# Performance work log

Hardware: AMD Instinct MI355X
Metric: run time of the kernel (lower is better)

Reference implementation:

```python
import jax, jax.numpy as jnp
import numpy as np

DROPOUT_P = 0.9  # module's self.dropout_p, training=True by default
DROPOUT_KEY = 42  # fixed key for deterministic reference


def setup_inputs() -> dict:
    key = jax.random.key(0)
    kq, kk, kv = jax.random.split(key, 3)
    B, H, S, D = 4, 16, 2048, 64
    q = jax.random.normal(kq, (B, H, S, D), dtype=jnp.float32)
    k = jax.random.normal(kk, (B, H, S, D), dtype=jnp.float32)
    v = jax.random.normal(kv, (B, H, S, D), dtype=jnp.float32)
    return {"q": q, "k": k, "v": v}


def reference(q, k, v):
    # qk = q @ k^T  -> [B,H,Sq,Skv]
    qk = jnp.einsum("bhqd,bhkd->bhqk", q, k)
    # NOTE: module divides by v.size(-1)**-0.5, i.e. multiplies by sqrt(Dv)
    inv_scale_factor = v.shape[-1] ** (-0.5)
    scaled_qk = qk / inv_scale_factor
    softmax_qk = jax.nn.softmax(scaled_qk, axis=-1)
    # dropout with p=0.9, training=True; fixed key for determinism
    keep = jax.random.bernoulli(jax.random.key(DROPOUT_KEY), 1.0 - DROPOUT_P, softmax_qk.shape)
    dropout_qk = jnp.where(keep, softmax_qk / (1.0 - DROPOUT_P), 0.0)
    out = jnp.einsum("bhqk,bhkd->bhqd", dropout_qk, v)
    return out
```

## Files before the change

### kernel.cpp

```cpp
#include <hip/hip_runtime.h>


typedef short short8 __attribute__((ext_vector_type(8)));
typedef float floatx4 __attribute__((ext_vector_type(4)));

#define S_LEN 2048
#define D_DIM 64
#define BM 64
#define BN 64
#define NTILES (S_LEN / BN)
#define E_THR 1e-7f
#define MARG 2.025f
#define CAND_CAP 40
#define K_ELEMS (64 * S_LEN * D_DIM)
#define WS_NEEDED ((size_t)K_ELEMS * 4)
#define TILE_BYTES 16384
#define BH_BYTES (NTILES * TILE_BYTES)

__device__ __forceinline__ unsigned int rotl32(unsigned int x, int n) {
  return (x << n) | (x >> (32 - n));
}

__device__ __forceinline__ unsigned int threefry_42_xorfold(unsigned int idx) {
  const unsigned int ks1 = 42u, ks2 = 0x1BD11BF0u;
  unsigned int x0 = 0u;
  unsigned int x1 = idx + ks1;
#define TF4(a, b, c, d)                          \
  x0 += x1; x1 = rotl32(x1, a); x1 ^= x0;        \
  x0 += x1; x1 = rotl32(x1, b); x1 ^= x0;        \
  x0 += x1; x1 = rotl32(x1, c); x1 ^= x0;        \
  x0 += x1; x1 = rotl32(x1, d); x1 ^= x0;
  TF4(13, 15, 26, 6)
  x0 += ks1; x1 += ks2 + 1u;
  TF4(17, 29, 16, 24)
  x0 += ks2; x1 += 2u;
  TF4(13, 15, 26, 6)
  x1 += ks1 + 3u;
  TF4(17, 29, 16, 24)
  x0 += ks1; x1 += ks2 + 4u;
  TF4(13, 15, 26, 6)
  x0 += ks2; x1 += 5u;
#undef TF4
  return x0 ^ x1;
}

__device__ __forceinline__ void split4(float4 x, uint2* hp, uint2* lop) {
  const unsigned int u0 = __float_as_uint(x.x), u1 = __float_as_uint(x.y);
  const unsigned int u2 = __float_as_uint(x.z), u3 = __float_as_uint(x.w);
  hp->x = (u0 >> 16) | (u1 & 0xFFFF0000u);
  hp->y = (u2 >> 16) | (u3 & 0xFFFF0000u);
  const float l0 = x.x - __uint_as_float(u0 & 0xFFFF0000u);
  const float l1 = x.y - __uint_as_float(u1 & 0xFFFF0000u);
  const float l2 = x.z - __uint_as_float(u2 & 0xFFFF0000u);
  const float l3 = x.w - __uint_as_float(u3 & 0xFFFF0000u);
  lop->x = (__float_as_uint(l0) >> 16) | (__float_as_uint(l1) & 0xFFFF0000u);
  lop->y = (__float_as_uint(l2) >> 16) | (__float_as_uint(l3) & 0xFFFF0000u);
}

__device__ __forceinline__ void split8(const float* x, short8* hi, short8* lo) {
  union { short8 s; uint2 u[2]; } h, l;
  split4(*(const float4*)(x + 0), &h.u[0], &l.u[0]);
  split4(*(const float4*)(x + 4), &h.u[1], &l.u[1]);
  *hi = h.s; *lo = l.s;
}

__global__ void split_k_kernel(const float* __restrict__ k, unsigned char* __restrict__ ws) {
  const int c = blockIdx.x * 256 + threadIdx.x;
  const int bh = c >> 14;
  const int cc = c & 16383;
  const int srow = cc >> 3, col8 = cc & 7;
  const int tile = srow >> 6, row = srow & 63;
  const float* src = k + ((size_t)bh * S_LEN + srow) * D_DIM + col8 * 8;
  float b8[8];
  *(float4*)&b8[0] = *(const float4*)src;
  *(float4*)&b8[4] = *(const float4*)(src + 4);
  short8 h, l;
  split8(b8, &h, &l);
  unsigned char* dst = ws + (size_t)bh * BH_BYTES + tile * TILE_BYTES +
                       row * 128 + ((col8 * 16) ^ ((row & 7) << 4));
  *(short8*)dst = h;
  *(short8*)(dst + 8192) = l;
}

__global__ __launch_bounds__(256, 4) void attn_dropout_kernel(
    const float* __restrict__ q, const float* __restrict__ k,
    const float* __restrict__ v, float* __restrict__ out,
    const unsigned char* __restrict__ kws, int usews) {
  __shared__ uint4 Kbuf[1024];
  __shared__ float2 cand[BM][CAND_CAP];
  __shared__ int cnt[BM];
  __shared__ float rowm8[BM];

  const int t = threadIdx.x;
  const int w = t >> 6;
  const int m16 = t & 15;
  const int qd = (t & 63) >> 4;
  const int lane = t & 63;
  const int i0 = blockIdx.x * BM;
  const int bh = blockIdx.y;

  const float* Qg = q + ((size_t)bh * S_LEN + i0) * D_DIM;
  const float* Kg = k + (size_t)bh * S_LEN * D_DIM;
  const float* Vg = v + (size_t)bh * S_LEN * D_DIM;

  if (t < BM) cnt[t] = 0;

  short8 ah0, ah1, al0, al1;
  {
    const int arow = 16 * w + m16;
    float qbuf[8];
    *(float4*)&qbuf[0] = *(const float4*)(Qg + arow * D_DIM + qd * 8);
    *(float4*)&qbuf[4] = *(const float4*)(Qg + arow * D_DIM + qd * 8 + 4);
    split8(qbuf, &ah0, &al0);
    *(float4*)&qbuf[0] = *(const float4*)(Qg + arow * D_DIM + 32 + qd * 8);
    *(float4*)&qbuf[4] = *(const float4*)(Qg + arow * D_DIM + 32 + qd * 8 + 4);
    split8(qbuf, &ah1, &al1);
  }

  float mrow[4];
#pragma unroll
  for (int r = 0; r < 4; ++r) mrow[r] = -1e30f;

  const unsigned int bh_base = (unsigned int)bh * (unsigned int)(S_LEN * S_LEN);

  const int swz = (m16 & 7) << 4;
  const int b_lo = m16 * 128 + ((qd * 16) ^ swz);
  const int b_hi = m16 * 128 + ((qd * 16 + 64) ^ swz);

  auto compute_tile = [&](int j0) {
    const char* Kb = (const char*)&Kbuf[0];
    floatx4 acc[4];
#pragma unroll
    for (int jj = 0; jj < 4; ++jj) {
      short8 kh0 = *(const short8*)(Kb + jj * 2048 + b_lo);
      short8 kh1 = *(const short8*)(Kb + jj * 2048 + b_hi);
      short8 kl0 = *(const short8*)(Kb + 8192 + jj * 2048 + b_lo);
      short8 kl1 = *(const short8*)(Kb + 8192 + jj * 2048 + b_hi);
      floatx4 a = {0.f, 0.f, 0.f, 0.f};
      a = __builtin_amdgcn_mfma_f32_16x16x32_bf16(ah0, kh0, a, 0, 0, 0);
      a = __builtin_amdgcn_mfma_f32_16x16x32_bf16(ah1, kh1, a, 0, 0, 0);
      a = __builtin_amdgcn_mfma_f32_16x16x32_bf16(ah0, kl0, a, 0, 0, 0);
      a = __builtin_amdgcn_mfma_f32_16x16x32_bf16(ah1, kl1, a, 0, 0, 0);
      a = __builtin_amdgcn_mfma_f32_16x16x32_bf16(al0, kh0, a, 0, 0, 0);
      a = __builtin_amdgcn_mfma_f32_16x16x32_bf16(al1, kh1, a, 0, 0, 0);
      acc[jj] = a;
    }
#pragma unroll
    for (int r = 0; r < 4; ++r) {
      const float rl = fmaxf(fmaxf(acc[0][r], acc[1][r]), fmaxf(acc[2][r], acc[3][r]));
      const unsigned long long b = __ballot(rl > mrow[r] - MARG);
      if ((b >> (16 * qd)) & 0xFFFFull) {
        float rmx = rl;
#pragma unroll
        for (int off = 1; off < 16; off <<= 1)
          rmx = fmaxf(rmx, __shfl_xor(rmx, off, 16));
        const float mn = fmaxf(mrow[r], rmx);
        mrow[r] = mn;
        const float thr = mn - MARG;
        const int lrow = 16 * w + 4 * qd + r;
#pragma unroll
        for (int jj = 0; jj < 4; ++jj) {
          if (acc[jj][r] > thr) {
            const int slot = atomicAdd(&cnt[lrow], 1);
            if (slot < CAND_CAP)
              cand[lrow][slot] = make_float2(8.f * acc[jj][r],
                                             __uint_as_float((unsigned int)(j0 + 16 * jj + m16)));
          }
        }
      }
    }
  };

  if (usews) {
    const uint4* gk = (const uint4*)(kws + (size_t)bh * BH_BYTES) + (w * 256 + lane);
    uint4* lp = &Kbuf[0] + (w * 256 + lane);
    uint4 r0 = gk[0], r1 = gk[64], r2 = gk[128], r3 = gk[192];

    for (int tile = 0; tile < NTILES; ++tile) {
      __syncthreads();
      lp[0] = r0; lp[64] = r1; lp[128] = r2; lp[192] = r3;
      __syncthreads();
      if (tile + 1 < NTILES) {
        const uint4* gp = gk + (size_t)(tile + 1) * 1024;
        r0 = gp[0]; r1 = gp[64]; r2 = gp[128]; r3 = gp[192];
      }
      compute_tile(tile * BN);
    }
  } else {
    for (int tile = 0; tile < NTILES; ++tile) {
      const int j0 = tile * BN;
      __syncthreads();
#pragma unroll
      for (int rr = 0; rr < 4; ++rr) {
        const int c = t + 256 * rr;
        const int row = c >> 4, c4 = (c & 15) * 4;
        float4 x = *(const float4*)(Kg + (size_t)(j0 + row) * D_DIM + c4);
        uint2 h, l;
        split4(x, &h, &l);
        const int bcol = c4 * 2;
        const int dst = row * 128 + ((bcol & ~15) ^ ((row & 7) << 4)) + (bcol & 15);
        char* Kb0 = (char*)&Kbuf[0];
        *(uint2*)(Kb0 + dst) = h;
        *(uint2*)(Kb0 + 8192 + dst) = l;
      }
      __syncthreads();
      compute_tile(j0);
    }
  }

  if (m16 == 0) {
#pragma unroll
    for (int r = 0; r < 4; ++r) rowm8[16 * w + 4 * qd + r] = 8.f * mrow[r];
  }
  __syncthreads();

#pragma unroll 1
  for (int ri = 0; ri < 16; ++ri) {
    const int lrow = 16 * w + ri;
    const int ncand = min(cnt[lrow], CAND_CAP);
    const float m8 = rowm8[lrow];

    float e = 0.f;
    unsigned int col = 0u;
    if (lane < ncand) {
      const float2 cd = cand[lrow][lane];
      col = __float_as_uint(cd.y);
      e = __expf(cd.x - m8);
    }

    float lsum = e;
#pragma unroll
    for (int off = 1; off < 64; off <<= 1) lsum += __shfl_xor(lsum, off);
    lsum = fmaxf(lsum, 1e-30f);

    float p = 0.f;
    if (e > E_THR) {
      const unsigned int idx = bh_base +
          (unsigned int)(i0 + lrow) * (unsigned int)S_LEN + col;
      const unsigned int rr = threefry_42_xorfold(idx);
      const float u = __uint_as_float((rr >> 9) | 0x3f800000u) - 1.0f;
      if (u < 0.1f) p = e;
    }

    float o = 0.f;
    unsigned long long kb = __ballot(p != 0.f);
    while (kb) {
      const int src = __builtin_ctzll(kb);
      kb &= kb - 1;
      const float pb = __shfl(p, src);
      const int cb = __shfl((int)col, src);
      o = fmaf(pb, Vg[(size_t)cb * D_DIM + lane], o);
    }

    const float scale = 10.0f / lsum;
    out[((size_t)bh * S_LEN + i0 + lrow) * D_DIM + lane] = o * scale;
  }
}

extern "C" void kernel_launch(void* const* d_in, const int* in_sizes, int n_in,
                              void* d_out, int out_size, void* d_ws, size_t ws_size,
                              hipStream_t stream) {
  (void)in_sizes; (void)n_in;
  const float* q = (const float*)d_in[0];
  const float* k = (const float*)d_in[1];
  const float* v = (const float*)d_in[2];
  float* out = (float*)d_out;

  unsigned char* kws = (unsigned char*)d_ws;
  const int usews = (ws_size >= WS_NEEDED) ? 1 : 0;

  if (usews) {
    split_k_kernel<<<K_ELEMS / 8 / 256, 256, 0, stream>>>(k, kws);
  }
  dim3 grid(S_LEN / BM, 64);
  attn_dropout_kernel<<<grid, 256, 0, stream>>>(q, k, v, out, kws, usews);

  if (hipGetLastError() != hipSuccess) {
    hipMemsetAsync(d_out, 0x42, (size_t)out_size * sizeof(float), stream);
  }
}
```

Baseline: 302.7 us.

## Stream K low halves from global in MFMA layout, halve LDS to raise occupancy

```diff
diff --git a/kernel.cpp b/kernel.cpp
--- a/kernel.cpp
+++ b/kernel.cpp
@@ -76,18 +76,20 @@
   *(float4*)&b8[4] = *(const float4*)(src + 4);
   short8 h, l;
   split8(b8, &h, &l);
-  unsigned char* dst = ws + (size_t)bh * BH_BYTES + tile * TILE_BYTES +
-                       row * 128 + ((col8 * 16) ^ ((row & 7) << 4));
-  *(short8*)dst = h;
-  *(short8*)(dst + 8192) = l;
-}
-
-__global__ __launch_bounds__(256, 4) void attn_dropout_kernel(
+  unsigned char* base = ws + (size_t)bh * BH_BYTES + tile * TILE_BYTES;
+  *(short8*)(base + row * 128 + ((col8 * 16) ^ ((row & 7) << 4))) = h;
+  const int jj = row >> 4, kk = col8 >> 2;
+  const int lane = (col8 & 3) * 16 + (row & 15);
+  *(short8*)(base + 8192 + jj * 2048 + kk * 1024 + lane * 16) = l;
+}
+
+__global__ __launch_bounds__(256, 6) void attn_dropout_kernel(
     const float* __restrict__ q, const float* __restrict__ k,
     const float* __restrict__ v, float* __restrict__ out,
     const unsigned char* __restrict__ kws, int usews) {
-  __shared__ uint4 Kbuf[1024];
-  __shared__ float2 cand[BM][CAND_CAP];
+  __shared__ uint4 Kbuf[512];
+  __shared__ float candv[BM][CAND_CAP];
+  __shared__ unsigned short candc[BM][CAND_CAP];
   __shared__ int cnt[BM];
   __shared__ float rowm8[BM];
 
@@ -127,24 +129,7 @@
   const int b_lo = m16 * 128 + ((qd * 16) ^ swz);
   const int b_hi = m16 * 128 + ((qd * 16 + 64) ^ swz);
 
-  auto compute_tile = [&](int j0) {
-    const char* Kb = (const char*)&Kbuf[0];
-    floatx4 acc[4];
-#pragma unroll
-    for (int jj = 0; jj < 4; ++jj) {
-      short8 kh0 = *(const short8*)(Kb + jj * 2048 + b_lo);
-      short8 kh1 = *(const short8*)(Kb + jj * 2048 + b_hi);
-      short8 kl0 = *(const short8*)(Kb + 8192 + jj * 2048 + b_lo);
-      short8 kl1 = *(const short8*)(Kb + 8192 + jj * 2048 + b_hi);
-      floatx4 a = {0.f, 0.f, 0.f, 0.f};
-      a = __builtin_amdgcn_mfma_f32_16x16x32_bf16(ah0, kh0, a, 0, 0, 0);
-      a = __builtin_amdgcn_mfma_f32_16x16x32_bf16(ah1, kh1, a, 0, 0, 0);
-      a = __builtin_amdgcn_mfma_f32_16x16x32_bf16(ah0, kl0, a, 0, 0, 0);
-      a = __builtin_amdgcn_mfma_f32_16x16x32_bf16(ah1, kl1, a, 0, 0, 0);
-      a = __builtin_amdgcn_mfma_f32_16x16x32_bf16(al0, kh0, a, 0, 0, 0);
-      a = __builtin_amdgcn_mfma_f32_16x16x32_bf16(al1, kh1, a, 0, 0, 0);
-      acc[jj] = a;
-    }
+  auto do_stats = [&](const floatx4* acc, int j0) {
 #pragma unroll
     for (int r = 0; r < 4; ++r) {
       const float rl = fmaxf(fmaxf(acc[0][r], acc[1][r]), fmaxf(acc[2][r], acc[3][r]));
@@ -162,9 +147,10 @@
         for (int jj = 0; jj < 4; ++jj) {
           if (acc[jj][r] > thr) {
             const int slot = atomicAdd(&cnt[lrow], 1);
-            if (slot < CAND_CAP)
-              cand[lrow][slot] = make_float2(8.f * acc[jj][r],
-                                             __uint_as_float((unsigned int)(j0 + 16 * jj + m16)));
+            if (slot < CAND_CAP) {
+              candv[lrow][slot] = 8.f * acc[jj][r];
+              candc[lrow][slot] = (unsigned short)(j0 + 16 * jj + m16);
+            }
           }
         }
       }
@@ -172,39 +158,63 @@
   };
 
   if (usews) {
-    const uint4* gk = (const uint4*)(kws + (size_t)bh * BH_BYTES) + (w * 256 + lane);
-    uint4* lp = &Kbuf[0] + (w * 256 + lane);
-    uint4 r0 = gk[0], r1 = gk[64], r2 = gk[128], r3 = gk[192];
+    const uint4* gk = (const uint4*)(kws + (size_t)bh * BH_BYTES) + t;
+    uint4* lp = &Kbuf[0] + t;
+    uint4 r0 = gk[0], r1 = gk[256];
 
     for (int tile = 0; tile < NTILES; ++tile) {
       __syncthreads();
-      lp[0] = r0; lp[64] = r1; lp[128] = r2; lp[192] = r3;
+      lp[0] = r0; lp[256] = r1;
       __syncthreads();
       if (tile + 1 < NTILES) {
         const uint4* gp = gk + (size_t)(tile + 1) * 1024;
-        r0 = gp[0]; r1 = gp[64]; r2 = gp[128]; r3 = gp[192];
-      }
-      compute_tile(tile * BN);
+        r0 = gp[0]; r1 = gp[256];
+      }
+      const char* Kb = (const char*)&Kbuf[0];
+      const char* lob = (const char*)kws + (size_t)bh * BH_BYTES + tile * TILE_BYTES + 8192;
+      floatx4 acc[4];
+#pragma unroll
+      for (int jj = 0; jj < 4; ++jj) {
+        short8 kl0 = *(const short8*)(lob + jj * 2048 + lane * 16);
+        short8 kl1 = *(const short8*)(lob + jj * 2048 + 1024 + lane * 16);
+        short8 kh0 = *(const short8*)(Kb + jj * 2048 + b_lo);
+        short8 kh1 = *(const short8*)(Kb + jj * 2048 + b_hi);
+        floatx4 a = {0.f, 0.f, 0.f, 0.f};
+        a = __builtin_amdgcn_mfma_f32_16x16x32_bf16(ah0, kh0, a, 0, 0, 0);
+        a = __builtin_amdgcn_mfma_f32_16x16x32_bf16(ah1, kh1, a, 0, 0, 0);
+        a = __builtin_amdgcn_mfma_f32_16x16x32_bf16(al0, kh0, a, 0, 0, 0);
+        a = __builtin_amdgcn_mfma_f32_16x16x32_bf16(al1, kh1, a, 0, 0, 0);
+        a = __builtin_amdgcn_mfma_f32_16x16x32_bf16(ah0, kl0, a, 0, 0, 0);
+        a = __builtin_amdgcn_mfma_f32_16x16x32_bf16(ah1, kl1, a, 0, 0, 0);
+        acc[jj] = a;
+      }
+      do_stats(acc, tile * BN);
     }
   } else {
+    __syncthreads();
     for (int tile = 0; tile < NTILES; ++tile) {
-      const int j0 = tile * BN;
-      __syncthreads();
-#pragma unroll
-      for (int rr = 0; rr < 4; ++rr) {
-        const int c = t + 256 * rr;
-        const int row = c >> 4, c4 = (c & 15) * 4;
-        float4 x = *(const float4*)(Kg + (size_t)(j0 + row) * D_DIM + c4);
-        uint2 h, l;
-        split4(x, &h, &l);
-        const int bcol = c4 * 2;
-        const int dst = row * 128 + ((bcol & ~15) ^ ((row & 7) << 4)) + (bcol & 15);
-        char* Kb0 = (char*)&Kbuf[0];
-        *(uint2*)(Kb0 + dst) = h;
-        *(uint2*)(Kb0 + 8192 + dst) = l;
-      }
-      __syncthreads();
-      compute_tile(j0);
+      floatx4 acc[4];
+#pragma unroll
+      for (int jj = 0; jj < 4; ++jj) {
+        const float* kp = Kg + (size_t)(tile * BN + 16 * jj + m16) * D_DIM + qd * 8;
+        float b8[8];
+        short8 kh0, kh1, kl0, kl1;
+        *(float4*)&b8[0] = *(const float4*)kp;
+        *(float4*)&b8[4] = *(const float4*)(kp + 4);
+        split8(b8, &kh0, &kl0);
+        *(float4*)&b8[0] = *(const float4*)(kp + 32);
+        *(float4*)&b8[4] = *(const float4*)(kp + 36);
+        split8(b8, &kh1, &kl1);
+        floatx4 a = {0.f, 0.f, 0.f, 0.f};
+        a = __builtin_amdgcn_mfma_f32_16x16x32_bf16(ah0, kh0, a, 0, 0, 0);
+        a = __builtin_amdgcn_mfma_f32_16x16x32_bf16(ah1, kh1, a, 0, 0, 0);
+        a = __builtin_amdgcn_mfma_f32_16x16x32_bf16(al0, kh0, a, 0, 0, 0);
+        a = __builtin_amdgcn_mfma_f32_16x16x32_bf16(al1, kh1, a, 0, 0, 0);
+        a = __builtin_amdgcn_mfma_f32_16x16x32_bf16(ah0, kl0, a, 0, 0, 0);
+        a = __builtin_amdgcn_mfma_f32_16x16x32_bf16(ah1, kl1, a, 0, 0, 0);
+        acc[jj] = a;
+      }
+      do_stats(acc, tile * BN);
     }
   }
 
@@ -223,9 +233,8 @@
     float e = 0.f;
     unsigned int col = 0u;
     if (lane < ncand) {
-      const float2 cd = cand[lrow][lane];
-      col = __float_as_uint(cd.y);
-      e = __expf(cd.x - m8);
+      col = candc[lrow][lane];
+      e = __expf(candv[lrow][lane] - m8);
     }
 
     float lsum = e;
```

Measured after the change: 298.2 us. Within noise of the previous version (-1.5%).
